# Kernel optimization log

Measured on AMD Instinct MI355X. Metric: run time of the kernel, lower is better.

Reference implementation:

```python
import jax, jax.numpy as jnp
import numpy as np

E, D_IN, H, D_OUT = 8, 6, 32, 2
B = 1048576

def setup_inputs() -> dict:
    key = jax.random.key(0)
    ks = jax.random.split(key, 11)
    s = lambda *sh: 1.0 / np.sqrt(sh[-2])  # glorot-ish scale
    x = jax.random.normal(ks[0], (B, D_IN), dtype=jnp.float32)
    # stacked expert weights
    W1 = jax.random.normal(ks[1], (E, D_IN, H), dtype=jnp.float32) * (1.0/np.sqrt(D_IN))
    b1 = jnp.zeros((E, H), dtype=jnp.float32)
    W2 = jax.random.normal(ks[2], (E, H, H), dtype=jnp.float32) * (1.0/np.sqrt(H))
    b2 = jnp.zeros((E, H), dtype=jnp.float32)
    W3 = jax.random.normal(ks[3], (E, H, D_OUT), dtype=jnp.float32) * (1.0/np.sqrt(H))
    b3 = jnp.zeros((E, D_OUT), dtype=jnp.float32)
    # gating network
    Wg1 = jax.random.normal(ks[4], (D_IN, H), dtype=jnp.float32) * (1.0/np.sqrt(D_IN))
    bg1 = jnp.zeros((H,), dtype=jnp.float32)
    Wg2 = jax.random.normal(ks[5], (H, E), dtype=jnp.float32) * (1.0/np.sqrt(H))
    bg2 = jnp.zeros((E,), dtype=jnp.float32)
    return {"x": x, "W1": W1, "b1": b1, "W2": W2, "b2": b2, "W3": W3, "b3": b3,
            "Wg1": Wg1, "bg1": bg1, "Wg2": Wg2, "bg2": bg2}

def reference(x, W1, b1, W2, b2, W3, b3, Wg1, bg1, Wg2, bg2):
    # gate: [B, E] softmax probs
    g = jax.nn.softmax(jax.nn.relu(x @ Wg1 + bg1) @ Wg2 + bg2, axis=-1)
    # all experts as batched GEMMs: h1, h2 [B, E, H]; y [B, E, 2]
    h1 = jax.nn.relu(jnp.einsum('bd,edh->beh', x, W1) + b1)
    h2 = jax.nn.relu(jnp.einsum('beh,ehk->bek', h1, W2) + b2)
    y = jnp.einsum('beh,eho->beo', h2, W3) + b3
    # gate-weighted sum over experts -> [B, 2]
    return jnp.einsum('be,beo->bo', g, y)
```

## Files before the change

kernel.cpp:

```cpp
#include <hip/hip_runtime.h>


typedef _Float16 half2_t __attribute__((ext_vector_type(2)));
typedef _Float16 half8_t __attribute__((ext_vector_type(8)));
typedef __fp16   fp16v2  __attribute__((ext_vector_type(2)));
typedef float  f32x16   __attribute__((ext_vector_type(16)));
typedef float  float4_t __attribute__((ext_vector_type(4)));
typedef float  float2_t __attribute__((ext_vector_type(2)));
typedef int    int4_t   __attribute__((ext_vector_type(4)));

#define MFMA32(A, B, C) __builtin_amdgcn_mfma_f32_32x32x16_f16((A), (B), (C), 0, 0, 0)

static constexpr int E_ = 8, DIN_ = 6, H_ = 32;

union H8U { half2_t h2[4]; half8_t h8; int4_t i4; };
union HI  { half2_t h; int i; };
union PKU { fp16v2 p; half2_t h; };
union C16 { f32x16 v; float4_t q[4]; };

__device__ __forceinline__ half2_t pkrtz(float a, float b) {
    PKU u; u.p = __builtin_amdgcn_cvt_pkrtz(a, b);
    return u.h;
}

__device__ __forceinline__ half2_t relu2(half2_t v) {
    const half2_t z = {(_Float16)0.0f, (_Float16)0.0f};
    return __builtin_elementwise_max(v, z);
}

__global__ __launch_bounds__(256)
__attribute__((amdgpu_waves_per_eu(2, 2)))
void moe_kernel(
    const float* __restrict__ x,  const float* __restrict__ W1, const float* __restrict__ b1,
    const float* __restrict__ W2, const float* __restrict__ b2, const float* __restrict__ W3,
    const float* __restrict__ b3, const float* __restrict__ Wg1, const float* __restrict__ bg1,
    const float* __restrict__ Wg2, const float* __restrict__ bg2,
    float* __restrict__ out, int nTok, int nTiles, int tilesPerWave)
{
    const int tid  = threadIdx.x;
    const int lane = tid & 63;
    const int m    = lane & 31;
    const int h    = lane >> 5;
    const int wv   = tid >> 6;
    const int gw   = (blockIdx.x << 2) + wv;

    __shared__ H8U w1img[E_][64];
    __shared__ H8U w2img[E_][2][64];
    __shared__ H8U a3img[E_][2][64];
    __shared__ float b2s[E_][H_];

    const float L2E = 1.44269504f;
    const half2_t h2z = pkrtz(0.f, 0.f);

    #pragma unroll
    for (int j = 0; j < 2; ++j) {
        const int e = wv * 2 + j;
        H8U w1v;
        if (h == 0) {
            w1v.h2[0] = pkrtz(W1[(e*DIN_+0)*H_+m], W1[(e*DIN_+1)*H_+m]);
            w1v.h2[1] = pkrtz(W1[(e*DIN_+2)*H_+m], W1[(e*DIN_+3)*H_+m]);
        } else {
            w1v.h2[0] = pkrtz(W1[(e*DIN_+4)*H_+m], W1[(e*DIN_+5)*H_+m]);
            w1v.h2[1] = pkrtz(b1[e*H_+m], 0.f);
        }
        w1v.h2[2] = h2z; w1v.h2[3] = h2z;
        w1img[e][lane] = w1v;

        const int o = m & 1;
        const bool alive = ((m >> 1) == e);
        #pragma unroll
        for (int b = 0; b < 2; ++b) {
            H8U w2v, a3v;
            #pragma unroll
            for (int p = 0; p < 4; ++p) {
                const int k0 = 16*b + 8*(p>>1) + 4*h + 2*(p&1);
                w2v.h2[p] = pkrtz(W2[(e*H_+k0)*H_+m], W2[(e*H_+k0+1)*H_+m]);
                a3v.h2[p] = alive ? pkrtz(W3[(e*H_+k0)*2+o], W3[(e*H_+k0+1)*2+o]) : h2z;
            }
            w2img[e][b][lane] = w2v;
            a3img[e][b][lane] = a3v;
        }
        if (lane < H_) b2s[e][lane] = b2[e*H_ + lane];
    }

    H8U G1;
    if (h == 0) {
        G1.h2[0] = pkrtz(Wg1[0*H_+m], Wg1[1*H_+m]);
        G1.h2[1] = pkrtz(Wg1[2*H_+m], Wg1[3*H_+m]);
    } else {
        G1.h2[0] = pkrtz(Wg1[4*H_+m], Wg1[5*H_+m]);
        G1.h2[1] = pkrtz(bg1[m], 0.f);
    }
    G1.h2[2] = h2z; G1.h2[3] = h2z;

    H8U G2[2];
    {
        const bool alive = (m < E_);
        #pragma unroll
        for (int b = 0; b < 2; ++b)
            #pragma unroll
            for (int p = 0; p < 4; ++p) {
                const int k0 = 16*b + 8*(p>>1) + 4*h + 2*(p&1);
                G2[b].h2[p] = alive ? pkrtz(Wg2[k0*E_+m]*L2E, Wg2[(k0+1)*E_+m]*L2E) : h2z;
            }
    }
    float4_t bg2F;
    #pragma unroll
    for (int r = 0; r < 4; ++r) bg2F[r] = bg2[4*h + r] * L2E;

    float b3P[8];
    #pragma unroll
    for (int r = 0; r < 8; ++r) b3P[r] = b3[(r&3) + 8*(r>>2) + 4*h];

    const f32x16 z16 = {0,0,0,0, 0,0,0,0, 0,0,0,0, 0,0,0,0};
    const float4_t z4 = {0.f, 0.f, 0.f, 0.f};

    __syncthreads();

    const int tile0 = gw * tilesPerWave;
    const int xo1 = h ? 4 : 0;
    const int xo2 = h ? 4 : 2;
    const float* xq = x + ((size_t)tile0 * 32 + m) * DIN_;
    float2_t la = {0.f, 0.f}, lb = {0.f, 0.f};
    if (tile0 < nTiles && (size_t)tile0 * 32 + m < (size_t)nTok) {
        la = *(const float2_t*)(xq + xo1);
        lb = *(const float2_t*)(xq + xo2);
    }
    HI onei; onei.h = pkrtz(1.f, 0.f);

    for (int it = 0; it < tilesPerWave; ++it) {
        const int tile = tile0 + it;
        if (tile >= nTiles) break;
        const bool tok = ((size_t)tile * 32 + m) < (size_t)nTok;

        H8U xB;
        xB.h2[0] = pkrtz(la[0], la[1]);
        { HI hb; hb.h = pkrtz(lb[0], lb[1]); HI se; se.i = h ? onei.i : hb.i; xB.h2[1] = se.h; }
        xB.h2[2] = h2z; xB.h2[3] = h2z;

        if (it + 1 < tilesPerWave && tile + 1 < nTiles) {
            const float* xn = xq + (size_t)(it + 1) * 32 * DIN_;
            if ((size_t)(tile + 1) * 32 + m < (size_t)nTok) {
                la = *(const float2_t*)(xn + xo1);
                lb = *(const float2_t*)(xn + xo2);
            }
        }

        f32x16 hg = MFMA32(G1.h8, xB.h8, z16);
        H8U uhlo, uhhi;
        #pragma unroll
        for (int i = 0; i < 4; ++i) {
            uhlo.h2[i] = relu2(pkrtz(hg[2*i],   hg[2*i+1]));
            uhhi.h2[i] = relu2(pkrtz(hg[8+2*i], hg[8+2*i+1]));
        }
        C16 gc; gc.q[0] = bg2F; gc.q[1] = z4; gc.q[2] = z4; gc.q[3] = z4;
        f32x16 gl = MFMA32(G2[0].h8, uhlo.h8, gc.v);
        gl = MFMA32(G2[1].h8, uhhi.h8, gl);

        float ex0 = __builtin_amdgcn_exp2f(gl[0]);
        float ex1 = __builtin_amdgcn_exp2f(gl[1]);
        float ex2 = __builtin_amdgcn_exp2f(gl[2]);
        float ex3 = __builtin_amdgcn_exp2f(gl[3]);
        float s = (ex0 + ex1) + (ex2 + ex3);
        s += __shfl_xor(s, 32);
        float rs = __builtin_amdgcn_rcpf(s);
        float sA = h ? ex0 : ex2, sB = h ? ex1 : ex3;
        HI sp; sp.h = pkrtz(sA, sB);
        HI rp; rp.i = __shfl_xor(sp.i, 32);
        float rA = (float)rp.h[0], rB = (float)rp.h[1];
        float wA = h ? rA : ex0, wB = h ? rB : ex1;
        float wC = h ? ex2 : rA, wD = h ? ex3 : rB;

        f32x16 Y = z16;
        #pragma unroll
        for (int e = 0; e < E_; ++e) {
            H8U a1; a1.i4 = w1img[e][lane].i4;
            f32x16 c1 = MFMA32(a1.h8, xB.h8, z16);
            H8U u1lo, u1hi;
            #pragma unroll
            for (int i = 0; i < 4; ++i) {
                u1lo.h2[i] = relu2(pkrtz(c1[2*i],   c1[2*i+1]));
                u1hi.h2[i] = relu2(pkrtz(c1[8+2*i], c1[8+2*i+1]));
            }
            H8U a2lo, a2hi;
            a2lo.i4 = w2img[e][0][lane].i4;
            a2hi.i4 = w2img[e][1][lane].i4;
            C16 bc;
            bc.q[0] = *(const float4_t*)&b2s[e][4*h];
            bc.q[1] = *(const float4_t*)&b2s[e][8 + 4*h];
            bc.q[2] = *(const float4_t*)&b2s[e][16 + 4*h];
            bc.q[3] = *(const float4_t*)&b2s[e][24 + 4*h];
            f32x16 c2 = MFMA32(a2lo.h8, u1lo.h8, bc.v);
            c2 = MFMA32(a2hi.h8, u1hi.h8, c2);
            H8U u2lo, u2hi;
            #pragma unroll
            for (int i = 0; i < 4; ++i) {
                u2lo.h2[i] = relu2(pkrtz(c2[2*i],   c2[2*i+1]));
                u2hi.h2[i] = relu2(pkrtz(c2[8+2*i], c2[8+2*i+1]));
            }
            H8U a3lo, a3hi;
            a3lo.i4 = a3img[e][0][lane].i4;
            a3hi.i4 = a3img[e][1][lane].i4;
            Y = MFMA32(a3lo.h8, u2lo.h8, Y);
            Y = MFMA32(a3hi.h8, u2hi.h8, Y);
        }

        float p0 = wA*(Y[0]+b3P[0]) + wB*(Y[2]+b3P[2]) + wC*(Y[4]+b3P[4]) + wD*(Y[6]+b3P[6]);
        float p1 = wA*(Y[1]+b3P[1]) + wB*(Y[3]+b3P[3]) + wC*(Y[5]+b3P[5]) + wD*(Y[7]+b3P[7]);
        p0 += __shfl_xor(p0, 32);
        p1 += __shfl_xor(p1, 32);
        if (h == 0 && tok) {
            float2_t ov = {p0 * rs, p1 * rs};
            *(float2_t*)(out + ((size_t)tile * 32 + m) * 2) = ov;
        }
    }
}

extern "C" void kernel_launch(void* const* d_in, const int* in_sizes, int n_in,
                              void* d_out, int out_size, void* d_ws, size_t ws_size,
                              hipStream_t stream) {
    const float* x   = (const float*)d_in[0];
    const float* W1  = (const float*)d_in[1];
    const float* b1  = (const float*)d_in[2];
    const float* W2  = (const float*)d_in[3];
    const float* b2  = (const float*)d_in[4];
    const float* W3  = (const float*)d_in[5];
    const float* b3  = (const float*)d_in[6];
    const float* Wg1 = (const float*)d_in[7];
    const float* bg1 = (const float*)d_in[8];
    const float* Wg2 = (const float*)d_in[9];
    const float* bg2 = (const float*)d_in[10];
    float* out = (float*)d_out;

    const int B      = in_sizes[0] / DIN_;
    const int nTiles = (B + 31) / 32;
    const int blocks = 512;
    const int wavesTotal = blocks * 4;
    const int tpw = (nTiles + wavesTotal - 1) / wavesTotal;

    moe_kernel<<<blocks, 256, 0, stream>>>(x, W1, b1, W2, b2, W3, b3,
                                           Wg1, bg1, Wg2, bg2, out, B, nTiles, tpw);
}
```

Baseline: 131.1 us.

## Process two token tiles per iteration to share expert weight LDS loads

Each wave now handles two 32-token tiles per loop iteration. Each expert's weight fragments are read from LDS once and used for both tiles, which interleaves independent MFMA chains. The gate weights and biases move from registers into LDS and are reloaded through volatile reads each iteration, presumably to relieve register pressure. The b3 bias is folded into the Y accumulator initialisation. The cost is a larger live set (two accumulators plus prefetched inputs), and tilesPerWave not being a multiple of two relies on the bounds checks.

```diff
diff --git a/kernel.cpp b/kernel.cpp
--- a/kernel.cpp
+++ b/kernel.cpp
@@ -11,7 +11,7 @@
 
 #define MFMA32(A, B, C) __builtin_amdgcn_mfma_f32_32x32x16_f16((A), (B), (C), 0, 0, 0)
 
-static constexpr int E_ = 8, DIN_ = 6, H_ = 32;
+static constexpr int E_ = 8, DIN_ = 6, H_ = 32, TB_ = 2;
 
 union H8U { half2_t h2[4]; half8_t h8; int4_t i4; };
 union HI  { half2_t h; int i; };
@@ -47,7 +47,11 @@
     __shared__ H8U w1img[E_][64];
     __shared__ H8U w2img[E_][2][64];
     __shared__ H8U a3img[E_][2][64];
-    __shared__ float b2s[E_][H_];
+    __shared__ __align__(16) float b2s[E_][H_];
+    __shared__ H8U g1s[64];
+    __shared__ H8U g2s[2][64];
+    __shared__ __align__(16) float b3s[16];
+    __shared__ __align__(16) float bg2s[8];
 
     const float L2E = 1.44269504f;
     const half2_t h2z = pkrtz(0.f, 0.f);
@@ -83,34 +87,32 @@
         if (lane < H_) b2s[e][lane] = b2[e*H_ + lane];
     }
 
-    H8U G1;
-    if (h == 0) {
-        G1.h2[0] = pkrtz(Wg1[0*H_+m], Wg1[1*H_+m]);
-        G1.h2[1] = pkrtz(Wg1[2*H_+m], Wg1[3*H_+m]);
-    } else {
-        G1.h2[0] = pkrtz(Wg1[4*H_+m], Wg1[5*H_+m]);
-        G1.h2[1] = pkrtz(bg1[m], 0.f);
-    }
-    G1.h2[2] = h2z; G1.h2[3] = h2z;
-
-    H8U G2[2];
-    {
+    if (wv == 0) {
+        H8U g1v;
+        if (h == 0) {
+            g1v.h2[0] = pkrtz(Wg1[0*H_+m], Wg1[1*H_+m]);
+            g1v.h2[1] = pkrtz(Wg1[2*H_+m], Wg1[3*H_+m]);
+        } else {
+            g1v.h2[0] = pkrtz(Wg1[4*H_+m], Wg1[5*H_+m]);
+            g1v.h2[1] = pkrtz(bg1[m], 0.f);
+        }
+        g1v.h2[2] = h2z; g1v.h2[3] = h2z;
+        g1s[lane] = g1v;
+
         const bool alive = (m < E_);
         #pragma unroll
-        for (int b = 0; b < 2; ++b)
+        for (int b = 0; b < 2; ++b) {
+            H8U g2v;
             #pragma unroll
             for (int p = 0; p < 4; ++p) {
                 const int k0 = 16*b + 8*(p>>1) + 4*h + 2*(p&1);
-                G2[b].h2[p] = alive ? pkrtz(Wg2[k0*E_+m]*L2E, Wg2[(k0+1)*E_+m]*L2E) : h2z;
-            }
-    }
-    float4_t bg2F;
-    #pragma unroll
-    for (int r = 0; r < 4; ++r) bg2F[r] = bg2[4*h + r] * L2E;
-
-    float b3P[8];
-    #pragma unroll
-    for (int r = 0; r < 8; ++r) b3P[r] = b3[(r&3) + 8*(r>>2) + 4*h];
+                g2v.h2[p] = alive ? pkrtz(Wg2[k0*E_+m]*L2E, Wg2[(k0+1)*E_+m]*L2E) : h2z;
+            }
+            g2s[b][lane] = g2v;
+        }
+        if (lane < 16) b3s[lane] = b3[lane];
+        if (lane < E_) bg2s[lane] = bg2[lane] * L2E;
+    }
 
     const f32x16 z16 = {0,0,0,0, 0,0,0,0, 0,0,0,0, 0,0,0,0};
     const float4_t z4 = {0.f, 0.f, 0.f, 0.f};
@@ -121,97 +123,133 @@
     const int xo1 = h ? 4 : 0;
     const int xo2 = h ? 4 : 2;
     const float* xq = x + ((size_t)tile0 * 32 + m) * DIN_;
-    float2_t la = {0.f, 0.f}, lb = {0.f, 0.f};
-    if (tile0 < nTiles && (size_t)tile0 * 32 + m < (size_t)nTok) {
-        la = *(const float2_t*)(xq + xo1);
-        lb = *(const float2_t*)(xq + xo2);
+    float2_t la[TB_], lb[TB_];
+    #pragma unroll
+    for (int u = 0; u < TB_; ++u) {
+        la[u] = float2_t{0.f, 0.f};
+        lb[u] = float2_t{0.f, 0.f};
+        if (tile0 + u < nTiles && (size_t)(tile0 + u) * 32 + m < (size_t)nTok) {
+            la[u] = *(const float2_t*)(xq + (size_t)u * 32 * DIN_ + xo1);
+            lb[u] = *(const float2_t*)(xq + (size_t)u * 32 * DIN_ + xo2);
+        }
     }
     HI onei; onei.h = pkrtz(1.f, 0.f);
 
-    for (int it = 0; it < tilesPerWave; ++it) {
-        const int tile = tile0 + it;
-        if (tile >= nTiles) break;
-        const bool tok = ((size_t)tile * 32 + m) < (size_t)nTok;
-
-        H8U xB;
-        xB.h2[0] = pkrtz(la[0], la[1]);
-        { HI hb; hb.h = pkrtz(lb[0], lb[1]); HI se; se.i = h ? onei.i : hb.i; xB.h2[1] = se.h; }
-        xB.h2[2] = h2z; xB.h2[3] = h2z;
-
-        if (it + 1 < tilesPerWave && tile + 1 < nTiles) {
-            const float* xn = xq + (size_t)(it + 1) * 32 * DIN_;
-            if ((size_t)(tile + 1) * 32 + m < (size_t)nTok) {
-                la = *(const float2_t*)(xn + xo1);
-                lb = *(const float2_t*)(xn + xo2);
-            }
-        }
-
-        f32x16 hg = MFMA32(G1.h8, xB.h8, z16);
-        H8U uhlo, uhhi;
-        #pragma unroll
-        for (int i = 0; i < 4; ++i) {
-            uhlo.h2[i] = relu2(pkrtz(hg[2*i],   hg[2*i+1]));
-            uhhi.h2[i] = relu2(pkrtz(hg[8+2*i], hg[8+2*i+1]));
-        }
-        C16 gc; gc.q[0] = bg2F; gc.q[1] = z4; gc.q[2] = z4; gc.q[3] = z4;
-        f32x16 gl = MFMA32(G2[0].h8, uhlo.h8, gc.v);
-        gl = MFMA32(G2[1].h8, uhhi.h8, gl);
-
-        float ex0 = __builtin_amdgcn_exp2f(gl[0]);
-        float ex1 = __builtin_amdgcn_exp2f(gl[1]);
-        float ex2 = __builtin_amdgcn_exp2f(gl[2]);
-        float ex3 = __builtin_amdgcn_exp2f(gl[3]);
-        float s = (ex0 + ex1) + (ex2 + ex3);
-        s += __shfl_xor(s, 32);
-        float rs = __builtin_amdgcn_rcpf(s);
-        float sA = h ? ex0 : ex2, sB = h ? ex1 : ex3;
-        HI sp; sp.h = pkrtz(sA, sB);
-        HI rp; rp.i = __shfl_xor(sp.i, 32);
-        float rA = (float)rp.h[0], rB = (float)rp.h[1];
-        float wA = h ? rA : ex0, wB = h ? rB : ex1;
-        float wC = h ? ex2 : rA, wD = h ? ex3 : rB;
-
-        f32x16 Y = z16;
+    for (int it = 0; it < tilesPerWave; it += TB_) {
+        const int tbase = tile0 + it;
+        if (tbase >= nTiles) break;
+
+        H8U g1v;  g1v.i4  = *(const volatile int4_t*)&g1s[lane].i4;
+        H8U g2v0; g2v0.i4 = *(const volatile int4_t*)&g2s[0][lane].i4;
+        H8U g2v1; g2v1.i4 = *(const volatile int4_t*)&g2s[1][lane].i4;
+        float4_t bgq  = *(const volatile float4_t*)&bg2s[4*h];
+        float4_t b3q0 = *(const volatile float4_t*)&b3s[4*h];
+        float4_t b3q1 = *(const volatile float4_t*)&b3s[8 + 4*h];
+
+        H8U xB[TB_];
+        #pragma unroll
+        for (int u = 0; u < TB_; ++u) {
+            xB[u].h2[0] = pkrtz(la[u][0], la[u][1]);
+            HI hb; hb.h = pkrtz(lb[u][0], lb[u][1]);
+            HI se; se.i = h ? onei.i : hb.i;
+            xB[u].h2[1] = se.h;
+            xB[u].h2[2] = h2z; xB[u].h2[3] = h2z;
+        }
+
+        if (it + TB_ < tilesPerWave) {
+            const float* xn = xq + (size_t)(it + TB_) * 32 * DIN_;
+            #pragma unroll
+            for (int u = 0; u < TB_; ++u) {
+                if (tbase + TB_ + u < nTiles &&
+                    (size_t)(tbase + TB_ + u) * 32 + m < (size_t)nTok) {
+                    la[u] = *(const float2_t*)(xn + (size_t)u * 32 * DIN_ + xo1);
+                    lb[u] = *(const float2_t*)(xn + (size_t)u * 32 * DIN_ + xo2);
+                }
+            }
+        }
+
+        float wA[TB_], wB[TB_], wC[TB_], wD[TB_], rs[TB_];
+        #pragma unroll
+        for (int u = 0; u < TB_; ++u) {
+            f32x16 hg = MFMA32(g1v.h8, xB[u].h8, z16);
+            H8U uhlo, uhhi;
+            #pragma unroll
+            for (int i = 0; i < 4; ++i) {
+                uhlo.h2[i] = relu2(pkrtz(hg[2*i],   hg[2*i+1]));
+                uhhi.h2[i] = relu2(pkrtz(hg[8+2*i], hg[8+2*i+1]));
+            }
+            C16 gc; gc.q[0] = bgq; gc.q[1] = z4; gc.q[2] = z4; gc.q[3] = z4;
+            f32x16 gl = MFMA32(g2v0.h8, uhlo.h8, gc.v);
+            gl = MFMA32(g2v1.h8, uhhi.h8, gl);
+
+            float ex0 = __builtin_amdgcn_exp2f(gl[0]);
+            float ex1 = __builtin_amdgcn_exp2f(gl[1]);
+            float ex2 = __builtin_amdgcn_exp2f(gl[2]);
+            float ex3 = __builtin_amdgcn_exp2f(gl[3]);
+            float s = (ex0 + ex1) + (ex2 + ex3);
+            s += __shfl_xor(s, 32);
+            rs[u] = __builtin_amdgcn_rcpf(s);
+            float sA = h ? ex0 : ex2, sB = h ? ex1 : ex3;
+            HI sp; sp.h = pkrtz(sA, sB);
+            HI rp; rp.i = __shfl_xor(sp.i, 32);
+            float rA = (float)rp.h[0], rB = (float)rp.h[1];
+            wA[u] = h ? rA : ex0; wB[u] = h ? rB : ex1;
+            wC[u] = h ? ex2 : rA; wD[u] = h ? ex3 : rB;
+        }
+
+        f32x16 Y[TB_];
+        #pragma unroll
+        for (int u = 0; u < TB_; ++u) {
+            C16 yc; yc.q[0] = b3q0; yc.q[1] = b3q1; yc.q[2] = z4; yc.q[3] = z4;
+            Y[u] = yc.v;
+        }
         #pragma unroll
         for (int e = 0; e < E_; ++e) {
-            H8U a1; a1.i4 = w1img[e][lane].i4;
-            f32x16 c1 = MFMA32(a1.h8, xB.h8, z16);
-            H8U u1lo, u1hi;
-            #pragma unroll
-            for (int i = 0; i < 4; ++i) {
-                u1lo.h2[i] = relu2(pkrtz(c1[2*i],   c1[2*i+1]));
-                u1hi.h2[i] = relu2(pkrtz(c1[8+2*i], c1[8+2*i+1]));
-            }
-            H8U a2lo, a2hi;
-            a2lo.i4 = w2img[e][0][lane].i4;
-            a2hi.i4 = w2img[e][1][lane].i4;
+            H8U a1;   a1.i4   = w1img[e][lane].i4;
+            H8U a2lo; a2lo.i4 = w2img[e][0][lane].i4;
+            H8U a2hi; a2hi.i4 = w2img[e][1][lane].i4;
+            H8U a3lo; a3lo.i4 = a3img[e][0][lane].i4;
+            H8U a3hi; a3hi.i4 = a3img[e][1][lane].i4;
             C16 bc;
             bc.q[0] = *(const float4_t*)&b2s[e][4*h];
             bc.q[1] = *(const float4_t*)&b2s[e][8 + 4*h];
             bc.q[2] = *(const float4_t*)&b2s[e][16 + 4*h];
             bc.q[3] = *(const float4_t*)&b2s[e][24 + 4*h];
-            f32x16 c2 = MFMA32(a2lo.h8, u1lo.h8, bc.v);
-            c2 = MFMA32(a2hi.h8, u1hi.h8, c2);
-            H8U u2lo, u2hi;
-            #pragma unroll
-            for (int i = 0; i < 4; ++i) {
-                u2lo.h2[i] = relu2(pkrtz(c2[2*i],   c2[2*i+1]));
-                u2hi.h2[i] = relu2(pkrtz(c2[8+2*i], c2[8+2*i+1]));
-            }
-            H8U a3lo, a3hi;
-            a3lo.i4 = a3img[e][0][lane].i4;
-            a3hi.i4 = a3img[e][1][lane].i4;
-            Y = MFMA32(a3lo.h8, u2lo.h8, Y);
-            Y = MFMA32(a3hi.h8, u2hi.h8, Y);
-        }
-
-        float p0 = wA*(Y[0]+b3P[0]) + wB*(Y[2]+b3P[2]) + wC*(Y[4]+b3P[4]) + wD*(Y[6]+b3P[6]);
-        float p1 = wA*(Y[1]+b3P[1]) + wB*(Y[3]+b3P[3]) + wC*(Y[5]+b3P[5]) + wD*(Y[7]+b3P[7]);
-        p0 += __shfl_xor(p0, 32);
-        p1 += __shfl_xor(p1, 32);
-        if (h == 0 && tok) {
-            float2_t ov = {p0 * rs, p1 * rs};
-            *(float2_t*)(out + ((size_t)tile * 32 + m) * 2) = ov;
+
+            #pragma unroll
+            for (int u = 0; u < TB_; ++u) {
+                f32x16 c1 = MFMA32(a1.h8, xB[u].h8, z16);
+                H8U u1lo, u1hi;
+                #pragma unroll
+                for (int i = 0; i < 4; ++i) {
+                    u1lo.h2[i] = relu2(pkrtz(c1[2*i],   c1[2*i+1]));
+                    u1hi.h2[i] = relu2(pkrtz(c1[8+2*i], c1[8+2*i+1]));
+                }
+                f32x16 c2 = MFMA32(a2lo.h8, u1lo.h8, bc.v);
+                c2 = MFMA32(a2hi.h8, u1hi.h8, c2);
+                H8U u2lo, u2hi;
+                #pragma unroll
+                for (int i = 0; i < 4; ++i) {
+                    u2lo.h2[i] = relu2(pkrtz(c2[2*i],   c2[2*i+1]));
+                    u2hi.h2[i] = relu2(pkrtz(c2[8+2*i], c2[8+2*i+1]));
+                }
+                Y[u] = MFMA32(a3lo.h8, u2lo.h8, Y[u]);
+                Y[u] = MFMA32(a3hi.h8, u2hi.h8, Y[u]);
+            }
+        }
+
+        #pragma unroll
+        for (int u = 0; u < TB_; ++u) {
+            const int tile = tbase + u;
+            float p0 = wA[u]*Y[u][0] + wB[u]*Y[u][2] + wC[u]*Y[u][4] + wD[u]*Y[u][6];
+            float p1 = wA[u]*Y[u][1] + wB[u]*Y[u][3] + wC[u]*Y[u][5] + wD[u]*Y[u][7];
+            p0 += __shfl_xor(p0, 32);
+            p1 += __shfl_xor(p1, 32);
+            const bool tok = tile < nTiles && ((size_t)tile * 32 + m) < (size_t)nTok;
+            if (h == 0 && tok) {
+                float2_t ov = {p0 * rs[u], p1 * rs[u]};
+                *(float2_t*)(out + ((size_t)tile * 32 + m) * 2) = ov;
+            }
         }
     }
 }
```

Result: slower. 135.1 us (+3.1%).

## Move gate weights and biases to LDS to raise occupancy to three waves

Applied to the files above, without the earlier changes.

Gate weights Wg1/Wg2, bg2 and b3 now live in shared memory and are reloaded through volatile LDS reads each tile instead of being held in registers. This frees registers so the kernel can target three waves per EU, and the grid grows from 512 to 768 blocks to match. b3 is folded into the initial Y accumulator, and the per-expert LDS loads are hoisted ahead of the MFMA chain. The trade-off is extra LDS traffic per tile and the chance of spills under the tighter register budget.

```diff
diff --git a/kernel.cpp b/kernel.cpp
--- a/kernel.cpp
+++ b/kernel.cpp
@@ -29,7 +29,7 @@
 }
 
 __global__ __launch_bounds__(256)
-__attribute__((amdgpu_waves_per_eu(2, 2)))
+__attribute__((amdgpu_waves_per_eu(3, 3)))
 void moe_kernel(
     const float* __restrict__ x,  const float* __restrict__ W1, const float* __restrict__ b1,
     const float* __restrict__ W2, const float* __restrict__ b2, const float* __restrict__ W3,
@@ -47,7 +47,11 @@
     __shared__ H8U w1img[E_][64];
     __shared__ H8U w2img[E_][2][64];
     __shared__ H8U a3img[E_][2][64];
-    __shared__ float b2s[E_][H_];
+    __shared__ __align__(16) float b2s[E_][H_];
+    __shared__ H8U g1s[64];
+    __shared__ H8U g2s[2][64];
+    __shared__ __align__(16) float b3s[16];
+    __shared__ __align__(16) float bg2s[8];
 
     const float L2E = 1.44269504f;
     const half2_t h2z = pkrtz(0.f, 0.f);
@@ -83,34 +87,32 @@
         if (lane < H_) b2s[e][lane] = b2[e*H_ + lane];
     }
 
-    H8U G1;
-    if (h == 0) {
-        G1.h2[0] = pkrtz(Wg1[0*H_+m], Wg1[1*H_+m]);
-        G1.h2[1] = pkrtz(Wg1[2*H_+m], Wg1[3*H_+m]);
-    } else {
-        G1.h2[0] = pkrtz(Wg1[4*H_+m], Wg1[5*H_+m]);
-        G1.h2[1] = pkrtz(bg1[m], 0.f);
-    }
-    G1.h2[2] = h2z; G1.h2[3] = h2z;
-
-    H8U G2[2];
-    {
+    if (wv == 0) {
+        H8U g1v;
+        if (h == 0) {
+            g1v.h2[0] = pkrtz(Wg1[0*H_+m], Wg1[1*H_+m]);
+            g1v.h2[1] = pkrtz(Wg1[2*H_+m], Wg1[3*H_+m]);
+        } else {
+            g1v.h2[0] = pkrtz(Wg1[4*H_+m], Wg1[5*H_+m]);
+            g1v.h2[1] = pkrtz(bg1[m], 0.f);
+        }
+        g1v.h2[2] = h2z; g1v.h2[3] = h2z;
+        g1s[lane] = g1v;
+
         const bool alive = (m < E_);
         #pragma unroll
-        for (int b = 0; b < 2; ++b)
+        for (int b = 0; b < 2; ++b) {
+            H8U g2v;
             #pragma unroll
             for (int p = 0; p < 4; ++p) {
                 const int k0 = 16*b + 8*(p>>1) + 4*h + 2*(p&1);
-                G2[b].h2[p] = alive ? pkrtz(Wg2[k0*E_+m]*L2E, Wg2[(k0+1)*E_+m]*L2E) : h2z;
-            }
-    }
-    float4_t bg2F;
-    #pragma unroll
-    for (int r = 0; r < 4; ++r) bg2F[r] = bg2[4*h + r] * L2E;
-
-    float b3P[8];
-    #pragma unroll
-    for (int r = 0; r < 8; ++r) b3P[r] = b3[(r&3) + 8*(r>>2) + 4*h];
+                g2v.h2[p] = alive ? pkrtz(Wg2[k0*E_+m]*L2E, Wg2[(k0+1)*E_+m]*L2E) : h2z;
+            }
+            g2s[b][lane] = g2v;
+        }
+        if (lane < 16) b3s[lane] = b3[lane];
+        if (lane < E_) bg2s[lane] = bg2[lane] * L2E;
+    }
 
     const f32x16 z16 = {0,0,0,0, 0,0,0,0, 0,0,0,0, 0,0,0,0};
     const float4_t z4 = {0.f, 0.f, 0.f, 0.f};
@@ -133,6 +135,13 @@
         if (tile >= nTiles) break;
         const bool tok = ((size_t)tile * 32 + m) < (size_t)nTok;
 
+        H8U g1v;  g1v.i4  = *(const volatile int4_t*)&g1s[lane].i4;
+        H8U g2v0; g2v0.i4 = *(const volatile int4_t*)&g2s[0][lane].i4;
+        H8U g2v1; g2v1.i4 = *(const volatile int4_t*)&g2s[1][lane].i4;
+        float4_t bgq  = *(const volatile float4_t*)&bg2s[4*h];
+        float4_t b3q0 = *(const volatile float4_t*)&b3s[4*h];
+        float4_t b3q1 = *(const volatile float4_t*)&b3s[8 + 4*h];
+
         H8U xB;
         xB.h2[0] = pkrtz(la[0], la[1]);
         { HI hb; hb.h = pkrtz(lb[0], lb[1]); HI se; se.i = h ? onei.i : hb.i; xB.h2[1] = se.h; }
@@ -146,16 +155,16 @@
             }
         }
 
-        f32x16 hg = MFMA32(G1.h8, xB.h8, z16);
+        f32x16 hg = MFMA32(g1v.h8, xB.h8, z16);
         H8U uhlo, uhhi;
         #pragma unroll
         for (int i = 0; i < 4; ++i) {
             uhlo.h2[i] = relu2(pkrtz(hg[2*i],   hg[2*i+1]));
             uhhi.h2[i] = relu2(pkrtz(hg[8+2*i], hg[8+2*i+1]));
         }
-        C16 gc; gc.q[0] = bg2F; gc.q[1] = z4; gc.q[2] = z4; gc.q[3] = z4;
-        f32x16 gl = MFMA32(G2[0].h8, uhlo.h8, gc.v);
-        gl = MFMA32(G2[1].h8, uhhi.h8, gl);
+        C16 gc; gc.q[0] = bgq; gc.q[1] = z4; gc.q[2] = z4; gc.q[3] = z4;
+        f32x16 gl = MFMA32(g2v0.h8, uhlo.h8, gc.v);
+        gl = MFMA32(g2v1.h8, uhhi.h8, gl);
 
         float ex0 = __builtin_amdgcn_exp2f(gl[0]);
         float ex1 = __builtin_amdgcn_exp2f(gl[1]);
@@ -171,25 +180,28 @@
         float wA = h ? rA : ex0, wB = h ? rB : ex1;
         float wC = h ? ex2 : rA, wD = h ? ex3 : rB;
 
-        f32x16 Y = z16;
+        f32x16 Y;
+        { C16 yc; yc.q[0] = b3q0; yc.q[1] = b3q1; yc.q[2] = z4; yc.q[3] = z4; Y = yc.v; }
         #pragma unroll
         for (int e = 0; e < E_; ++e) {
-            H8U a1; a1.i4 = w1img[e][lane].i4;
-            f32x16 c1 = MFMA32(a1.h8, xB.h8, z16);
-            H8U u1lo, u1hi;
-            #pragma unroll
-            for (int i = 0; i < 4; ++i) {
-                u1lo.h2[i] = relu2(pkrtz(c1[2*i],   c1[2*i+1]));
-                u1hi.h2[i] = relu2(pkrtz(c1[8+2*i], c1[8+2*i+1]));
-            }
-            H8U a2lo, a2hi;
-            a2lo.i4 = w2img[e][0][lane].i4;
-            a2hi.i4 = w2img[e][1][lane].i4;
+            H8U a1;   a1.i4   = w1img[e][lane].i4;
+            H8U a2lo; a2lo.i4 = w2img[e][0][lane].i4;
+            H8U a2hi; a2hi.i4 = w2img[e][1][lane].i4;
+            H8U a3lo; a3lo.i4 = a3img[e][0][lane].i4;
+            H8U a3hi; a3hi.i4 = a3img[e][1][lane].i4;
             C16 bc;
             bc.q[0] = *(const float4_t*)&b2s[e][4*h];
             bc.q[1] = *(const float4_t*)&b2s[e][8 + 4*h];
             bc.q[2] = *(const float4_t*)&b2s[e][16 + 4*h];
             bc.q[3] = *(const float4_t*)&b2s[e][24 + 4*h];
+
+            f32x16 c1 = MFMA32(a1.h8, xB.h8, z16);
+            H8U u1lo, u1hi;
+            #pragma unroll
+            for (int i = 0; i < 4; ++i) {
+                u1lo.h2[i] = relu2(pkrtz(c1[2*i],   c1[2*i+1]));
+                u1hi.h2[i] = relu2(pkrtz(c1[8+2*i], c1[8+2*i+1]));
+            }
             f32x16 c2 = MFMA32(a2lo.h8, u1lo.h8, bc.v);
             c2 = MFMA32(a2hi.h8, u1hi.h8, c2);
             H8U u2lo, u2hi;
@@ -198,15 +210,12 @@
                 u2lo.h2[i] = relu2(pkrtz(c2[2*i],   c2[2*i+1]));
                 u2hi.h2[i] = relu2(pkrtz(c2[8+2*i], c2[8+2*i+1]));
             }
-            H8U a3lo, a3hi;
-            a3lo.i4 = a3img[e][0][lane].i4;
-            a3hi.i4 = a3img[e][1][lane].i4;
             Y = MFMA32(a3lo.h8, u2lo.h8, Y);
             Y = MFMA32(a3hi.h8, u2hi.h8, Y);
         }
 
-        float p0 = wA*(Y[0]+b3P[0]) + wB*(Y[2]+b3P[2]) + wC*(Y[4]+b3P[4]) + wD*(Y[6]+b3P[6]);
-        float p1 = wA*(Y[1]+b3P[1]) + wB*(Y[3]+b3P[3]) + wC*(Y[5]+b3P[5]) + wD*(Y[7]+b3P[7]);
+        float p0 = wA*Y[0] + wB*Y[2] + wC*Y[4] + wD*Y[6];
+        float p1 = wA*Y[1] + wB*Y[3] + wC*Y[5] + wD*Y[7];
         p0 += __shfl_xor(p0, 32);
         p1 += __shfl_xor(p1, 32);
         if (h == 0 && tok) {
@@ -234,7 +243,7 @@
 
     const int B      = in_sizes[0] / DIN_;
     const int nTiles = (B + 31) / 32;
-    const int blocks = 512;
+    const int blocks = 768;
     const int wavesTotal = blocks * 4;
     const int tpw = (nTiles + wavesTotal - 1) / wavesTotal;
 
```

Result: no change. 131.2 us (+0.1%).
